# Kernel tuning notes

Hardware: AMD Instinct MI355X
Metric: run time of the kernel (lower is better)

## Reference

```python
import jax, jax.numpy as jnp
import numpy as np

EPS = 1e-6  # F.normalize eps

N, C, H, W = 2, 64, 64, 64
HEADS, DK, DV = 2, 64, 32


def setup_inputs() -> dict:
    key = jax.random.key(0)
    ks = jax.random.split(key, 9)
    w = lambda k, sh: jax.random.normal(k, sh, jnp.float32) * 0.05
    return {
        "x":  jax.random.normal(ks[0], (N, C, H, W), jnp.float32),
        "Wq": w(ks[1], (HEADS, DK, C)), "bq": w(ks[2], (HEADS, DK)),
        "Wk": w(ks[3], (HEADS, DK, C)), "bk": w(ks[4], (HEADS, DK)),
        "Wv": w(ks[5], (HEADS, DV, C)), "bv": w(ks[6], (HEADS, DV)),
        "Wm": w(ks[7], (C, HEADS * DV)), "bm": w(ks[8], (C,)),
    }


def _l2norm(t):
    # F.normalize(dim=1) on [N, dk, L]; here heads are stacked: [N, h, dk, L], axis=2
    n = jnp.linalg.norm(t, axis=2, keepdims=True)
    return t / jnp.maximum(n, EPS)


def reference(x, Wq, bq, Wk, bk, Wv, bv, Wm, bm):
    n, c, h, w = x.shape
    L = h * w
    xf = x.reshape(n, c, L)  # 1x1 conv == pointwise channel GEMM; x_enc = x (no pos enc)
    Q = jnp.einsum('hkc,ncl->nhkl', Wq, xf) + bq[None, :, :, None]
    K = jnp.einsum('hkc,ncl->nhkl', Wk, xf) + bk[None, :, :, None]
    V = jnp.einsum('hvc,ncl->nhvl', Wv, xf) + bv[None, :, :, None]
    Q = _l2norm(Q)
    K = _l2norm(K)
    # cosine-similarity attention: contract over dk, softmax over keys
    A = jax.nn.softmax(jnp.einsum('nhkl,nhkm->nhlm', Q, K), axis=-1)  # [n,h,L,L]
    R = jnp.einsum('nhlm,nhvm->nhvl', A, V)  # [n,h,dv,L]
    Rc = R.reshape(n, -1, L)  # concat heads along channels
    out = jnp.einsum('oc,ncl->nol', Wm, Rc) + bm[None, :, None]
    return out.reshape(n, c, h, w) + x  # residual
```

## Files before the change

### kernel.cpp

```cpp
#include <hip/hip_runtime.h>
#include <cmath>


typedef __bf16 bf16x8 __attribute__((ext_vector_type(8)));
typedef __bf16 bf16x4 __attribute__((ext_vector_type(4)));
typedef float f4_t __attribute__((ext_vector_type(4)));

#define LQ 4096
#define NH 4
#define KS 8

__device__ inline f4_t mfma16(bf16x8 a, bf16x8 b, f4_t c) {
    return __builtin_amdgcn_mfma_f32_16x16x32_bf16(a, b, c, 0, 0, 0);
}

__global__ void k0_prep(const float* __restrict__ Wq, const float* __restrict__ bq,
                        const float* __restrict__ Wk, const float* __restrict__ bk,
                        const float* __restrict__ Wv, const float* __restrict__ bv,
                        __bf16* __restrict__ Wb, float* __restrict__ bb) {
    const int tid = threadIdx.x;
    const int row = blockIdx.x * 64 + (tid >> 2);
    const int c0  = (tid & 3) * 16;

    const float* wsrc;
    float bval;
    if (row < 128)      { wsrc = Wq + (size_t)row * 64;         bval = bq[row]; }
    else if (row < 256) { wsrc = Wk + (size_t)(row - 128) * 64; bval = bk[row - 128]; }
    else                { wsrc = Wv + (size_t)(row - 256) * 64; bval = bv[row - 256]; }

#pragma unroll
    for (int j = 0; j < 16; ++j)
        Wb[(size_t)row * 64 + c0 + j] = (__bf16)wsrc[c0 + j];
    if ((tid & 3) == 0) bb[row] = bval;
}

__global__ __launch_bounds__(256) void k1_qkv(
        const float* __restrict__ x,
        const __bf16* __restrict__ Wb, const float* __restrict__ bb,
        __bf16* __restrict__ Qb, __bf16* __restrict__ Kb,
        __bf16* __restrict__ Vtb) {
    const int tid  = threadIdx.x;
    const int lane = tid & 63;
    const int w    = tid >> 6;
    const int quad = lane >> 4;
    const int l15  = lane & 15;
    const int lt   = blockIdx.x;
    const int n    = blockIdx.y;
    const int l0   = lt * 32;

    __shared__ __bf16 xl[32][72];

    {
        const int c0 = tid >> 5, l = tid & 31;
#pragma unroll
        for (int i = 0; i < 8; ++i) {
            const int c = c0 + i * 8;
            xl[l][c] = (__bf16)x[((size_t)n * 64 + c) * LQ + l0 + l];
        }
    }

    bf16x8 af[4][2], av[2];
#pragma unroll
    for (int t = 0; t < 4; ++t)
#pragma unroll
        for (int kh = 0; kh < 2; ++kh)
            af[t][kh] = *(const bf16x8*)(Wb +
                (size_t)(w * 64 + t * 16 + l15) * 64 + kh * 32 + quad * 8);
#pragma unroll
    for (int kh = 0; kh < 2; ++kh)
        av[kh] = *(const bf16x8*)(Wb +
            (size_t)(256 + w * 16 + l15) * 64 + kh * 32 + quad * 8);

    f4_t binit[4], bvinit;
#pragma unroll
    for (int t = 0; t < 4; ++t)
#pragma unroll
        for (int r = 0; r < 4; ++r)
            binit[t][r] = bb[w * 64 + t * 16 + quad * 4 + r];
#pragma unroll
    for (int r = 0; r < 4; ++r)
        bvinit[r] = bb[256 + w * 16 + quad * 4 + r];

    __syncthreads();

    f4_t acc[4][2], vacc[2];
#pragma unroll
    for (int lsub = 0; lsub < 2; ++lsub) {
        bf16x8 bf0 = *(const bf16x8*)&xl[lsub * 16 + l15][quad * 8];
        bf16x8 bf1 = *(const bf16x8*)&xl[lsub * 16 + l15][32 + quad * 8];
#pragma unroll
        for (int t = 0; t < 4; ++t) {
            f4_t a = mfma16(af[t][0], bf0, binit[t]);
            acc[t][lsub] = mfma16(af[t][1], bf1, a);
        }
        f4_t va = mfma16(av[0], bf0, bvinit);
        vacc[lsub] = mfma16(av[1], bf1, va);
    }

    const int nh = n * 2 + (w & 1);
    __bf16* dst  = (w < 2) ? Qb : Kb;
#pragma unroll
    for (int lsub = 0; lsub < 2; ++lsub) {
        float ss = 0.f;
#pragma unroll
        for (int t = 0; t < 4; ++t)
#pragma unroll
            for (int r = 0; r < 4; ++r)
                ss = fmaf(acc[t][lsub][r], acc[t][lsub][r], ss);
        ss += __shfl_xor(ss, 16, 64);
        ss += __shfl_xor(ss, 32, 64);
        const float rn = 1.0f / fmaxf(sqrtf(ss), 1e-6f);

        const int l = l0 + lsub * 16 + l15;
#pragma unroll
        for (int t = 0; t < 4; ++t) {
            bf16x4 pk;
#pragma unroll
            for (int r = 0; r < 4; ++r) pk[r] = (__bf16)(acc[t][lsub][r] * rn);
            const int kc = t * 2 + (quad >> 1);
            *(bf16x4*)(dst + ((size_t)(nh * 8 + kc) * LQ + l) * 8 + (quad & 1) * 4) = pk;
        }
#pragma unroll
        for (int r = 0; r < 4; ++r) {
            const int vrow = w * 16 + quad * 4 + r;
            Vtb[(size_t)(n * 64 + vrow) * LQ + l] = (__bf16)vacc[lsub][r];
        }
    }
}

__global__ __launch_bounds__(256, 4) void k2_attn(
        const __bf16* __restrict__ Qb, const __bf16* __restrict__ Kb,
        const __bf16* __restrict__ Vtb,
        float* __restrict__ numP, float* __restrict__ denP) {
    const int tid  = threadIdx.x;
    const int lane = tid & 63;
    const int wave = tid >> 6;
    const int quad = lane >> 4;
    const int l15  = lane & 15;
    const int nh   = blockIdx.y;
    const int ks   = blockIdx.z;
    const int qbase = blockIdx.x * 128 + wave * 32;
    const int kbase = ks * 512;

    __shared__ __bf16 Kl[2][2048];
    __shared__ __bf16 P[4][2][16][40];

    const f4_t fzero = {0.f, 0.f, 0.f, 0.f};

    const int s_kc = ((tid >> 6) & 1) * 4 + ((tid >> 4) & 3);
    const int s_l  = ((tid >> 7) << 4) | (tid & 15);
    const __bf16* s_src = Kb + ((size_t)(nh * 8 + s_kc) * LQ + kbase + s_l) * 8;

    bf16x8 qf[2][2];
#pragma unroll
    for (int qt = 0; qt < 2; ++qt)
#pragma unroll
        for (int kh = 0; kh < 2; ++kh)
            qf[qt][kh] = *(const bf16x8*)(Qb +
                ((size_t)(nh * 8 + kh * 4 + quad) * LQ + qbase + qt * 16 + l15) * 8);

    f4_t racc[2][2];
#pragma unroll
    for (int a = 0; a < 2; ++a)
#pragma unroll
        for (int b = 0; b < 2; ++b) racc[a][b] = fzero;
    float den[2] = {0.f, 0.f};

    *(bf16x8*)&Kl[0][tid * 8] = *(const bf16x8*)s_src;
    __syncthreads();

    for (int ch = 0; ch < 16; ++ch) {
        const int cur = ch & 1;

        if (ch < 15)
            *(bf16x8*)&Kl[cur ^ 1][tid * 8] =
                *(const bf16x8*)(s_src + (size_t)(ch + 1) * 32 * 8);

        const int kb = kbase + ch * 32;

        bf16x8 vf[2];
#pragma unroll
        for (int vt = 0; vt < 2; ++vt)
            vf[vt] = *(const bf16x8*)(Vtb +
                (size_t)(nh * 32 + vt * 16 + l15) * LQ + kb + quad * 8);

        bf16x8 kf[2][2];
#pragma unroll
        for (int kt = 0; kt < 2; ++kt)
#pragma unroll
            for (int kh = 0; kh < 2; ++kh)
                kf[kt][kh] = *(const bf16x8*)
                    &Kl[cur][(kt * 128 + kh * 64 + quad * 16 + l15) * 8];

        f4_t s[2][2];
#pragma unroll
        for (int qt = 0; qt < 2; ++qt)
#pragma unroll
            for (int kt = 0; kt < 2; ++kt) {
                f4_t t = mfma16(kf[kt][0], qf[qt][0], fzero);
                s[qt][kt] = mfma16(kf[kt][1], qf[qt][1], t);
            }

#pragma unroll
        for (int qt = 0; qt < 2; ++qt)
#pragma unroll
            for (int kt = 0; kt < 2; ++kt) {
                bf16x4 pv;
                float d = 0.f;
#pragma unroll
                for (int r = 0; r < 4; ++r) {
                    float p = __expf(s[qt][kt][r]);
                    d += p;
                    pv[r] = (__bf16)p;
                }
                den[qt] += d;
                *(bf16x4*)&P[wave][qt][l15][kt * 16 + quad * 4] = pv;
            }

#pragma unroll
        for (int qt = 0; qt < 2; ++qt) {
            bf16x8 pf = *(const bf16x8*)&P[wave][qt][l15][quad * 8];
#pragma unroll
            for (int vt = 0; vt < 2; ++vt)
                racc[vt][qt] = mfma16(vf[vt], pf, racc[vt][qt]);
        }

        __syncthreads();
    }

#pragma unroll
    for (int qt = 0; qt < 2; ++qt) {
        den[qt] += __shfl_xor(den[qt], 16, 64);
        den[qt] += __shfl_xor(den[qt], 32, 64);
    }

    const size_t pb = (size_t)(nh * KS + ks) * LQ;
#pragma unroll
    for (int vt = 0; vt < 2; ++vt)
#pragma unroll
        for (int qt = 0; qt < 2; ++qt)
#pragma unroll
            for (int r = 0; r < 4; ++r)
                numP[(pb + qbase + qt * 16 + l15) * 32 + vt * 16 + quad * 4 + r]
                    = racc[vt][qt][r];

    if (lane < 16)
#pragma unroll
        for (int qt = 0; qt < 2; ++qt)
            denP[pb + qbase + qt * 16 + lane] = den[qt];
}

__global__ __launch_bounds__(256) void k3_out(
        const float* __restrict__ numP, const float* __restrict__ denP,
        const float* __restrict__ Wm, const float* __restrict__ bm,
        const float* __restrict__ x, float* __restrict__ out) {
    const int tid  = threadIdx.x;
    const int lane = tid & 63;
    const int wv   = tid >> 6;
    const int n    = blockIdx.x >> 6;
    const int lt   = blockIdx.x & 63;
    const int l0   = lt * 64;

    __shared__ float Rf[64][65];
    __shared__ float dinv[2][64];

    if (tid < 128) {
        const int hh = tid >> 6, li = tid & 63;
        float s = 0.f;
#pragma unroll
        for (int k = 0; k < KS; ++k)
            s += denP[(size_t)((n * 2 + hh) * KS + k) * LQ + l0 + li];
        dinv[hh][li] = 1.0f / s;
    }

    {
        const int v = tid & 31, lsub = tid >> 5;
#pragma unroll
        for (int hh = 0; hh < 2; ++hh) {
            const size_t base = (size_t)(n * 2 + hh) * KS * LQ;
#pragma unroll
            for (int i = 0; i < 8; ++i) {
                const int l = lsub + 8 * i;
                float s = 0.f;
#pragma unroll
                for (int k = 0; k < KS; ++k)
                    s += numP[(base + (size_t)k * LQ + l0 + l) * 32 + v];
                Rf[hh * 32 + v][l] = s;
            }
        }
    }
    __syncthreads();

    const float d0 = dinv[0][lane], d1 = dinv[1][lane];
    float rj[64];
#pragma unroll
    for (int j = 0; j < 64; ++j)
        rj[j] = Rf[j][lane] * (j < 32 ? d0 : d1);

    float acc[16];
#pragma unroll
    for (int oi = 0; oi < 16; ++oi) acc[oi] = bm[wv * 16 + oi];
#pragma unroll
    for (int oi = 0; oi < 16; ++oi) {
        const float* wr = Wm + (size_t)(wv * 16 + oi) * 64;
        float a = acc[oi];
#pragma unroll
        for (int j4 = 0; j4 < 16; ++j4) {
            f4_t t = *(const f4_t*)(wr + j4 * 4);
            a = fmaf(t[0], rj[j4 * 4 + 0], a);
            a = fmaf(t[1], rj[j4 * 4 + 1], a);
            a = fmaf(t[2], rj[j4 * 4 + 2], a);
            a = fmaf(t[3], rj[j4 * 4 + 3], a);
        }
        acc[oi] = a;
    }

#pragma unroll
    for (int oi = 0; oi < 16; ++oi) {
        const int o = wv * 16 + oi;
        const size_t idx = (size_t)(n * 64 + o) * LQ + l0 + lane;
        out[idx] = acc[oi] + x[idx];
    }
}

extern "C" void kernel_launch(void* const* d_in, const int* in_sizes, int n_in,
                              void* d_out, int out_size, void* d_ws, size_t ws_size,
                              hipStream_t stream) {
    const float* x  = (const float*)d_in[0];
    const float* Wq = (const float*)d_in[1];
    const float* bq = (const float*)d_in[2];
    const float* Wk = (const float*)d_in[3];
    const float* bk = (const float*)d_in[4];
    const float* Wv = (const float*)d_in[5];
    const float* bv = (const float*)d_in[6];
    const float* Wm = (const float*)d_in[7];
    const float* bm = (const float*)d_in[8];
    float* out = (float*)d_out;

    __bf16* Qb  = (__bf16*)d_ws;
    __bf16* Kb  = Qb + (size_t)NH * LQ * 64;
    __bf16* Vtb = Kb + (size_t)NH * LQ * 64;
    float*  numP = (float*)(Vtb + (size_t)NH * 32 * LQ);
    float*  denP = numP + (size_t)NH * KS * 32 * LQ;
    __bf16* Wb  = (__bf16*)(denP + (size_t)NH * KS * LQ);
    float*  bb  = (float*)(Wb + 320 * 64);

    k0_prep<<<dim3(5), dim3(256), 0, stream>>>(Wq, bq, Wk, bk, Wv, bv, Wb, bb);
    k1_qkv<<<dim3(128, 2), dim3(256), 0, stream>>>(x, Wb, bb, Qb, Kb, Vtb);
    k2_attn<<<dim3(32, NH, KS), dim3(256), 0, stream>>>(Qb, Kb, Vtb, numP, denP);
    k3_out<<<dim3(128), dim3(256), 0, stream>>>(numP, denP, Wm, bm, x, out);
}
```

Baseline: 120.6 us.

## Fuse weight prep into QKV, prefetch V, bf16 partials, exp2, finer out grid

Removes the separate weight-conversion kernel by converting fp32 weights to bf16 inside the QKV kernel. Folds log2(e) into the Q normalization so the attention kernel can call exp2 directly. Prefetches V fragments one chunk ahead. Stores the per-split numerator partials as bf16, which halves that traffic but loses some precision. The output kernel is regridded into smaller 16-column tiles with more blocks. Together these cut one launch, reduce intermediate memory traffic and hide V load latency.

Result: faster. 114.7 us (-4.9%).

```diff
diff --git a/kernel.cpp b/kernel.cpp
--- a/kernel.cpp
+++ b/kernel.cpp
@@ -14,29 +14,19 @@
     return __builtin_amdgcn_mfma_f32_16x16x32_bf16(a, b, c, 0, 0, 0);
 }
 
-__global__ void k0_prep(const float* __restrict__ Wq, const float* __restrict__ bq,
-                        const float* __restrict__ Wk, const float* __restrict__ bk,
-                        const float* __restrict__ Wv, const float* __restrict__ bv,
-                        __bf16* __restrict__ Wb, float* __restrict__ bb) {
-    const int tid = threadIdx.x;
-    const int row = blockIdx.x * 64 + (tid >> 2);
-    const int c0  = (tid & 3) * 16;
-
-    const float* wsrc;
-    float bval;
-    if (row < 128)      { wsrc = Wq + (size_t)row * 64;         bval = bq[row]; }
-    else if (row < 256) { wsrc = Wk + (size_t)(row - 128) * 64; bval = bk[row - 128]; }
-    else                { wsrc = Wv + (size_t)(row - 256) * 64; bval = bv[row - 256]; }
-
-#pragma unroll
-    for (int j = 0; j < 16; ++j)
-        Wb[(size_t)row * 64 + c0 + j] = (__bf16)wsrc[c0 + j];
-    if ((tid & 3) == 0) bb[row] = bval;
+__device__ inline bf16x8 cvt8(const float* p) {
+    f4_t a = *(const f4_t*)p, b = *(const f4_t*)(p + 4);
+    bf16x8 r;
+    r[0] = (__bf16)a[0]; r[1] = (__bf16)a[1]; r[2] = (__bf16)a[2]; r[3] = (__bf16)a[3];
+    r[4] = (__bf16)b[0]; r[5] = (__bf16)b[1]; r[6] = (__bf16)b[2]; r[7] = (__bf16)b[3];
+    return r;
 }
 
 __global__ __launch_bounds__(256) void k1_qkv(
         const float* __restrict__ x,
-        const __bf16* __restrict__ Wb, const float* __restrict__ bb,
+        const float* __restrict__ Wq, const float* __restrict__ bq,
+        const float* __restrict__ Wk, const float* __restrict__ bk,
+        const float* __restrict__ Wv, const float* __restrict__ bv,
         __bf16* __restrict__ Qb, __bf16* __restrict__ Kb,
         __bf16* __restrict__ Vtb) {
     const int tid  = threadIdx.x;
@@ -59,27 +49,30 @@
         }
     }
 
+    const float* Wqk = (w < 2) ? Wq : Wk;
+    const float* bqk = (w < 2) ? bq : bk;
+    const int h = w & 1;
+
     bf16x8 af[4][2], av[2];
 #pragma unroll
     for (int t = 0; t < 4; ++t)
 #pragma unroll
         for (int kh = 0; kh < 2; ++kh)
-            af[t][kh] = *(const bf16x8*)(Wb +
-                (size_t)(w * 64 + t * 16 + l15) * 64 + kh * 32 + quad * 8);
+            af[t][kh] = cvt8(Wqk + (size_t)(h * 64 + t * 16 + l15) * 64
+                                  + kh * 32 + quad * 8);
 #pragma unroll
     for (int kh = 0; kh < 2; ++kh)
-        av[kh] = *(const bf16x8*)(Wb +
-            (size_t)(256 + w * 16 + l15) * 64 + kh * 32 + quad * 8);
+        av[kh] = cvt8(Wv + (size_t)(w * 16 + l15) * 64 + kh * 32 + quad * 8);
 
     f4_t binit[4], bvinit;
 #pragma unroll
     for (int t = 0; t < 4; ++t)
 #pragma unroll
         for (int r = 0; r < 4; ++r)
-            binit[t][r] = bb[w * 64 + t * 16 + quad * 4 + r];
+            binit[t][r] = bqk[h * 64 + t * 16 + quad * 4 + r];
 #pragma unroll
     for (int r = 0; r < 4; ++r)
-        bvinit[r] = bb[256 + w * 16 + quad * 4 + r];
+        bvinit[r] = bv[w * 16 + quad * 4 + r];
 
     __syncthreads();
 
@@ -97,8 +90,9 @@
         vacc[lsub] = mfma16(av[1], bf1, va);
     }
 
-    const int nh = n * 2 + (w & 1);
+    const int nh = n * 2 + h;
     __bf16* dst  = (w < 2) ? Qb : Kb;
+    const float post = (w < 2) ? 1.44269504f : 1.0f;
 #pragma unroll
     for (int lsub = 0; lsub < 2; ++lsub) {
         float ss = 0.f;
@@ -109,7 +103,7 @@
                 ss = fmaf(acc[t][lsub][r], acc[t][lsub][r], ss);
         ss += __shfl_xor(ss, 16, 64);
         ss += __shfl_xor(ss, 32, 64);
-        const float rn = 1.0f / fmaxf(sqrtf(ss), 1e-6f);
+        const float rn = post / fmaxf(sqrtf(ss), 1e-6f);
 
         const int l = l0 + lsub * 16 + l15;
 #pragma unroll
@@ -131,7 +125,7 @@
 __global__ __launch_bounds__(256, 4) void k2_attn(
         const __bf16* __restrict__ Qb, const __bf16* __restrict__ Kb,
         const __bf16* __restrict__ Vtb,
-        float* __restrict__ numP, float* __restrict__ denP) {
+        __bf16* __restrict__ numPb, float* __restrict__ denP) {
     const int tid  = threadIdx.x;
     const int lane = tid & 63;
     const int wave = tid >> 6;
@@ -166,23 +160,24 @@
         for (int b = 0; b < 2; ++b) racc[a][b] = fzero;
     float den[2] = {0.f, 0.f};
 
+    const __bf16* v_src = Vtb + (size_t)(nh * 32 + l15) * LQ + kbase + quad * 8;
+    bf16x8 vf_cur0 = *(const bf16x8*)v_src;
+    bf16x8 vf_cur1 = *(const bf16x8*)(v_src + (size_t)16 * LQ);
+
     *(bf16x8*)&Kl[0][tid * 8] = *(const bf16x8*)s_src;
     __syncthreads();
 
+#pragma unroll 2
     for (int ch = 0; ch < 16; ++ch) {
         const int cur = ch & 1;
 
-        if (ch < 15)
+        bf16x8 vf_nxt0, vf_nxt1;
+        if (ch < 15) {
             *(bf16x8*)&Kl[cur ^ 1][tid * 8] =
-                *(const bf16x8*)(s_src + (size_t)(ch + 1) * 32 * 8);
-
-        const int kb = kbase + ch * 32;
-
-        bf16x8 vf[2];
-#pragma unroll
-        for (int vt = 0; vt < 2; ++vt)
-            vf[vt] = *(const bf16x8*)(Vtb +
-                (size_t)(nh * 32 + vt * 16 + l15) * LQ + kb + quad * 8);
+                *(const bf16x8*)(s_src + (size_t)(ch + 1) * 256);
+            vf_nxt0 = *(const bf16x8*)(v_src + (ch + 1) * 32);
+            vf_nxt1 = *(const bf16x8*)(v_src + (size_t)16 * LQ + (ch + 1) * 32);
+        }
 
         bf16x8 kf[2][2];
 #pragma unroll
@@ -209,7 +204,7 @@
                 float d = 0.f;
 #pragma unroll
                 for (int r = 0; r < 4; ++r) {
-                    float p = __expf(s[qt][kt][r]);
+                    float p = __builtin_exp2f(s[qt][kt][r]);
                     d += p;
                     pv[r] = (__bf16)p;
                 }
@@ -220,12 +215,13 @@
 #pragma unroll
         for (int qt = 0; qt < 2; ++qt) {
             bf16x8 pf = *(const bf16x8*)&P[wave][qt][l15][quad * 8];
-#pragma unroll
-            for (int vt = 0; vt < 2; ++vt)
-                racc[vt][qt] = mfma16(vf[vt], pf, racc[vt][qt]);
+            racc[0][qt] = mfma16(vf_cur0, pf, racc[0][qt]);
+            racc[1][qt] = mfma16(vf_cur1, pf, racc[1][qt]);
         }
 
         __syncthreads();
+        vf_cur0 = vf_nxt0;
+        vf_cur1 = vf_nxt1;
     }
 
 #pragma unroll
@@ -238,11 +234,13 @@
 #pragma unroll
     for (int vt = 0; vt < 2; ++vt)
 #pragma unroll
-        for (int qt = 0; qt < 2; ++qt)
-#pragma unroll
-            for (int r = 0; r < 4; ++r)
-                numP[(pb + qbase + qt * 16 + l15) * 32 + vt * 16 + quad * 4 + r]
-                    = racc[vt][qt][r];
+        for (int qt = 0; qt < 2; ++qt) {
+            bf16x4 pk;
+#pragma unroll
+            for (int r = 0; r < 4; ++r) pk[r] = (__bf16)racc[vt][qt][r];
+            *(bf16x4*)(numPb + (pb + qbase + qt * 16 + l15) * 32
+                             + vt * 16 + quad * 4) = pk;
+        }
 
     if (lane < 16)
 #pragma unroll
@@ -251,21 +249,19 @@
 }
 
 __global__ __launch_bounds__(256) void k3_out(
-        const float* __restrict__ numP, const float* __restrict__ denP,
+        const __bf16* __restrict__ numPb, const float* __restrict__ denP,
         const float* __restrict__ Wm, const float* __restrict__ bm,
         const float* __restrict__ x, float* __restrict__ out) {
-    const int tid  = threadIdx.x;
-    const int lane = tid & 63;
-    const int wv   = tid >> 6;
-    const int n    = blockIdx.x >> 6;
-    const int lt   = blockIdx.x & 63;
-    const int l0   = lt * 64;
-
-    __shared__ float Rf[64][65];
-    __shared__ float dinv[2][64];
-
-    if (tid < 128) {
-        const int hh = tid >> 6, li = tid & 63;
+    const int tid = threadIdx.x;
+    const int lt  = blockIdx.x;
+    const int n   = blockIdx.y;
+    const int l0  = lt * 16;
+
+    __shared__ float Rf[64][17];
+    __shared__ float dinv[2][16];
+
+    if (tid < 32) {
+        const int hh = tid >> 4, li = tid & 15;
         float s = 0.f;
 #pragma unroll
         for (int k = 0; k < KS; ++k)
@@ -274,36 +270,33 @@
     }
 
     {
-        const int v = tid & 31, lsub = tid >> 5;
-#pragma unroll
-        for (int hh = 0; hh < 2; ++hh) {
-            const size_t base = (size_t)(n * 2 + hh) * KS * LQ;
-#pragma unroll
-            for (int i = 0; i < 8; ++i) {
-                const int l = lsub + 8 * i;
-                float s = 0.f;
-#pragma unroll
-                for (int k = 0; k < KS; ++k)
-                    s += numP[(base + (size_t)k * LQ + l0 + l) * 32 + v];
-                Rf[hh * 32 + v][l] = s;
-            }
+        const int v = tid & 31, lg = tid >> 5;
+        const int hh = lg & 1, lofs = lg >> 1;
+        const size_t base = (size_t)(n * 2 + hh) * KS * LQ;
+#pragma unroll
+        for (int i = 0; i < 4; ++i) {
+            const int l = lofs + 4 * i;
+            float s = 0.f;
+#pragma unroll
+            for (int k = 0; k < KS; ++k)
+                s += (float)numPb[(base + (size_t)k * LQ + l0 + l) * 32 + v];
+            Rf[hh * 32 + v][l] = s;
         }
     }
     __syncthreads();
 
-    const float d0 = dinv[0][lane], d1 = dinv[1][lane];
+    const int l = tid & 15, og = tid >> 4;
+    const float d0 = dinv[0][l], d1 = dinv[1][l];
     float rj[64];
 #pragma unroll
     for (int j = 0; j < 64; ++j)
-        rj[j] = Rf[j][lane] * (j < 32 ? d0 : d1);
-
-    float acc[16];
-#pragma unroll
-    for (int oi = 0; oi < 16; ++oi) acc[oi] = bm[wv * 16 + oi];
-#pragma unroll
-    for (int oi = 0; oi < 16; ++oi) {
-        const float* wr = Wm + (size_t)(wv * 16 + oi) * 64;
-        float a = acc[oi];
+        rj[j] = Rf[j][l] * (j < 32 ? d0 : d1);
+
+#pragma unroll
+    for (int oi = 0; oi < 4; ++oi) {
+        const int o = og * 4 + oi;
+        const float* wr = Wm + (size_t)o * 64;
+        float a = bm[o];
 #pragma unroll
         for (int j4 = 0; j4 < 16; ++j4) {
             f4_t t = *(const f4_t*)(wr + j4 * 4);
@@ -312,14 +305,8 @@
             a = fmaf(t[2], rj[j4 * 4 + 2], a);
             a = fmaf(t[3], rj[j4 * 4 + 3], a);
         }
-        acc[oi] = a;
-    }
-
-#pragma unroll
-    for (int oi = 0; oi < 16; ++oi) {
-        const int o = wv * 16 + oi;
-        const size_t idx = (size_t)(n * 64 + o) * LQ + l0 + lane;
-        out[idx] = acc[oi] + x[idx];
+        const size_t idx = (size_t)(n * 64 + o) * LQ + l0 + l;
+        out[idx] = a + x[idx];
     }
 }
 
@@ -337,16 +324,14 @@
     const float* bm = (const float*)d_in[8];
     float* out = (float*)d_out;
 
-    __bf16* Qb  = (__bf16*)d_ws;
-    __bf16* Kb  = Qb + (size_t)NH * LQ * 64;
-    __bf16* Vtb = Kb + (size_t)NH * LQ * 64;
-    float*  numP = (float*)(Vtb + (size_t)NH * 32 * LQ);
-    float*  denP = numP + (size_t)NH * KS * 32 * LQ;
-    __bf16* Wb  = (__bf16*)(denP + (size_t)NH * KS * LQ);
-    float*  bb  = (float*)(Wb + 320 * 64);
-
-    k0_prep<<<dim3(5), dim3(256), 0, stream>>>(Wq, bq, Wk, bk, Wv, bv, Wb, bb);
-    k1_qkv<<<dim3(128, 2), dim3(256), 0, stream>>>(x, Wb, bb, Qb, Kb, Vtb);
-    k2_attn<<<dim3(32, NH, KS), dim3(256), 0, stream>>>(Qb, Kb, Vtb, numP, denP);
-    k3_out<<<dim3(128), dim3(256), 0, stream>>>(numP, denP, Wm, bm, x, out);
-}
+    __bf16* Qb    = (__bf16*)d_ws;
+    __bf16* Kb    = Qb + (size_t)NH * LQ * 64;
+    __bf16* Vtb   = Kb + (size_t)NH * LQ * 64;
+    __bf16* numPb = Vtb + (size_t)NH * 32 * LQ;
+    float*  denP  = (float*)(numPb + (size_t)NH * KS * LQ * 32);
+
+    k1_qkv<<<dim3(128, 2), dim3(256), 0, stream>>>(x, Wq, bq, Wk, bk, Wv, bv,
+                                                   Qb, Kb, Vtb);
+    k2_attn<<<dim3(32, NH, KS), dim3(256), 0, stream>>>(Qb, Kb, Vtb, numPb, denP);
+    k3_out<<<dim3(256, 2), dim3(256), 0, stream>>>(numPb, denP, Wm, bm, x, out);
+}
```
